# Kernel tuning notes

Measured on AMD Instinct MI355X. Metric: run time of the kernel, lower is better.

## Reference

```python
import jax, jax.numpy as jnp
import numpy as np

MARGIN1 = 0.5
ALPHA = 1.0
GAMMA = 1.0
THETA = 0.1
K = 8  # num_instances per identity

N = 4096
D_FEA = 512
N_CLS = 751
D_SIDE = 1024


def setup_inputs() -> dict:
    key = jax.random.key(0)
    ks = jax.random.split(key, 5)
    return {
        "cls_fea": jax.random.normal(ks[0], (N, N_CLS), dtype=jnp.float32),
        "l2_side": jax.random.normal(ks[1], (N, D_SIDE), dtype=jnp.float32),
        "l3_side": jax.random.normal(ks[2], (N, D_SIDE), dtype=jnp.float32),
        "l4_side": jax.random.normal(ks[3], (N, D_SIDE), dtype=jnp.float32),
        "input_fea": jax.random.normal(ks[4], (N, D_FEA), dtype=jnp.float32),
        # PK sampling: exactly K consecutive samples per identity
        "targets": jnp.arange(N, dtype=jnp.int32) // K,
    }


def _rank_terms(dist, mask, n):
    """Vectorized replacement of the per-row rank-mining python loop."""
    j = jnp.arange(n)
    k = jnp.arange(K)

    def row(drow, mrow):
        order = jnp.argsort(drow)          # ascending distances
        sd = drow[order]                   # sort_dist
        pm = mrow[order]                   # positive mask in rank order
        # negatives that sneaked into the top-K ranks (== full_index leftovers)
        flag_neg = (~pm) & (j < K)
        # positives ranked outside top-K (== wrong_indice)
        flag_pos = pm & (j >= K)
        m = jnp.sum(flag_neg)              # left_wrong_num (counts match by construction)
        # wrong negatives in ascending rank order, padded to K slots
        neg_ord = jnp.argsort(jnp.where(flag_neg, j, j + n))[:K]
        # wrong positives in DESCENDING rank order (loop iterates reverse-sorted)
        pos_ord = jnp.argsort(jnp.where(flag_pos, -j, 1))[:K]
        wneg = sd[neg_ord]
        wpos = sd[pos_ord]
        valid = k < m
        most_wrong_neg = wneg[0]           # smallest wrong-negative distance
        ratio = (most_wrong_neg - wneg) / (most_wrong_neg + 1e-12)
        weight = (m - k).astype(sd.dtype) * jnp.exp(ratio)
        loss = jnp.sum(jnp.where(valid, weight * (wpos - wneg) + MARGIN1, 0.0))
        return loss, (m == 0)

    return jax.vmap(row)(dist, mask)


def reference(cls_fea, l2_side, l3_side, l4_side, input_fea, targets):
    n = input_fea.shape[0]
    # pairwise euclidean distance, clamped like torch .clamp(min=1e-12).sqrt()
    sq = jnp.sum(input_fea * input_fea, axis=1)
    d2 = sq[:, None] + sq[None, :] - 2.0 * (input_fea @ input_fea.T)
    dist = jnp.sqrt(jnp.maximum(d2, 1e-12))
    mask = targets[:, None] == targets[None, :]

    losses, corrects = _rank_terms(dist, mask, n)
    rank_loss = jnp.sum(losses) / n
    prec = jnp.mean(corrects.astype(jnp.float32))

    # cross entropy
    logp = jax.nn.log_softmax(cls_fea, axis=-1)
    xent = -jnp.mean(jnp.take_along_axis(logp, targets[:, None].astype(jnp.int32), axis=1))

    # side losses: frobenius norms of differences
    side_loss = jnp.sqrt(jnp.sum((l4_side - l2_side) ** 2)) + \
                jnp.sqrt(jnp.sum((l4_side - l3_side) ** 2))

    total = ALPHA * rank_loss + GAMMA * xent + THETA * side_loss

    # accuracy() helper (undefined in source): standard top-1 on input_fea vs targets
    acc = jnp.mean((jnp.argmax(input_fea, axis=1).astype(targets.dtype) == targets).astype(jnp.float32))
    prec2 = jnp.maximum(prec, acc)
    return total, prec2
```

## Files before the change

kernel.cpp:

```cpp
#include <hip/hip_runtime.h>
#include <hip/hip_bf16.h>
#include <math.h>

#define NROWS 4096
#define DFEA  512
#define NCLS  751
#define DSIDE 1024

typedef __attribute__((ext_vector_type(8))) short short8;
typedef __attribute__((ext_vector_type(4))) float f32x4;

__device__ __forceinline__ float wave_sum(float v) {
#pragma unroll
  for (int off = 32; off > 0; off >>= 1) v += __shfl_xor(v, off, 64);
  return v;
}

__device__ __forceinline__ void load_lds16(const void* g, void* l) {
  __builtin_amdgcn_global_load_lds((const __attribute__((address_space(1))) void*)g,
                                   (__attribute__((address_space(3))) void*)l, 16, 0, 0);
}

__device__ __forceinline__ void ins8(float t8[8], float x) {
#pragma unroll
  for (int q = 0; q < 8; ++q) {
    const float lo = fminf(t8[q], x);
    x = fmaxf(t8[q], x);
    t8[q] = lo;
  }
}

#define CE(x, i, j) { const float ce_lo = fminf(x[i], x[j]); x[j] = fmaxf(x[i], x[j]); x[i] = ce_lo; }
#define SORT8_STAGE(c) \
  CE(c, 0, 4) CE(c, 1, 5) CE(c, 2, 6) CE(c, 3, 7) \
  CE(c, 0, 2) CE(c, 1, 3) CE(c, 4, 6) CE(c, 5, 7) \
  CE(c, 0, 1) CE(c, 2, 3) CE(c, 4, 5) CE(c, 6, 7)

__device__ __forceinline__ void merge_sorted8(float a[8], int mask) {
  float b[8];
#pragma unroll
  for (int i = 0; i < 8; ++i) b[i] = __shfl_xor(a[i], mask, 64);
  float c[8];
#pragma unroll
  for (int i = 0; i < 8; ++i) c[i] = fminf(a[i], b[7 - i]);
  SORT8_STAGE(c)
#pragma unroll
  for (int i = 0; i < 8; ++i) a[i] = c[i];
}

__device__ __forceinline__ void merge8_local(float a[8], const float b[8]) {
  float c[8];
#pragma unroll
  for (int i = 0; i < 8; ++i) c[i] = fminf(a[i], b[7 - i]);
  SORT8_STAGE(c)
#pragma unroll
  for (int i = 0; i < 8; ++i) a[i] = c[i];
}

__device__ __forceinline__ unsigned short bf16bits(float v) {
  union { __hip_bfloat16 b; unsigned short u; } cv;
  cv.b = __float2bfloat16(v);
  return cv.u;
}

__global__ __launch_bounds__(256) void k_prep(const float* __restrict__ fea,
                                              const int* __restrict__ tgt,
                                              float* __restrict__ sq,
                                              float* __restrict__ pa,
                                              unsigned short* __restrict__ Fhi,
                                              unsigned short* __restrict__ Flo) {
  const int lane = threadIdx.x & 63;
  const int wid  = threadIdx.x >> 6;
  const int row  = blockIdx.x * 4 + wid;
  const float4* xr = (const float4*)(fea + (size_t)row * DFEA);
  ushort4* hr = (ushort4*)(Fhi + (size_t)row * DFEA);
  ushort4* lr = (ushort4*)(Flo + (size_t)row * DFEA);
  float s = 0.0f, bv = -1e30f;
  int bi = 0;
#pragma unroll
  for (int q = 0; q < 2; ++q) {
    const int i4 = q * 64 + lane;
    const float4 v = xr[i4];
    s += v.x * v.x + v.y * v.y + v.z * v.z + v.w * v.w;
    const int c0 = i4 * 4;
    if (v.x > bv) { bv = v.x; bi = c0; }
    if (v.y > bv) { bv = v.y; bi = c0 + 1; }
    if (v.z > bv) { bv = v.z; bi = c0 + 2; }
    if (v.w > bv) { bv = v.w; bi = c0 + 3; }
    ushort4 h, l;
    float hf;
    h.x = bf16bits(v.x); hf = __bfloat162float(__ushort_as_bfloat16(h.x)); l.x = bf16bits(v.x - hf);
    h.y = bf16bits(v.y); hf = __bfloat162float(__ushort_as_bfloat16(h.y)); l.y = bf16bits(v.y - hf);
    h.z = bf16bits(v.z); hf = __bfloat162float(__ushort_as_bfloat16(h.z)); l.z = bf16bits(v.z - hf);
    h.w = bf16bits(v.w); hf = __bfloat162float(__ushort_as_bfloat16(h.w)); l.w = bf16bits(v.w - hf);
    hr[i4] = h;
    lr[i4] = l;
  }
#pragma unroll
  for (int off = 32; off > 0; off >>= 1) {
    s += __shfl_xor(s, off, 64);
    const float ov = __shfl_xor(bv, off, 64);
    const int   oi = __shfl_xor(bi, off, 64);
    if (ov > bv || (ov == bv && oi < bi)) { bv = ov; bi = oi; }
  }
  __shared__ float red[4];
  if (lane == 0) {
    sq[row]  = s;
    red[wid] = (bi == tgt[row]) ? 1.0f : 0.0f;
  }
  __syncthreads();
  if (threadIdx.x == 0) pa[blockIdx.x] = red[0] + red[1] + red[2] + red[3];
}

__global__ __launch_bounds__(256) void k_gemm_mfma(const unsigned short* __restrict__ Fhi,
                                                   const unsigned short* __restrict__ Flo,
                                                   const float* __restrict__ sq,
                                                   float* __restrict__ posw,
                                                   float* __restrict__ part) {
  const int bid = blockIdx.x;
  int by = (int)((65.0f - sqrtf(4225.0f - 8.0f * (float)bid)) * 0.5f);
  while ((by + 1) * (65 - (by + 1)) / 2 <= bid) ++by;
  while (by * (65 - by) / 2 > bid) --by;
  const int bx = by + (bid - by * (65 - by) / 2);

  const int R0 = by * 128, C0 = bx * 128;
  const int tid = threadIdx.x;
  const int lane = tid & 63, wid = tid >> 6;
  const int wr = wid >> 1, wc = wid & 1;
  const int l15 = lane & 15, l4 = lane >> 4;

  __shared__ __attribute__((aligned(16))) char smem[37376];
  const __hip_bfloat16 (*As)[64] = (const __hip_bfloat16(*)[64])smem;
  const __hip_bfloat16 (*Bs)[64] = (const __hip_bfloat16(*)[64])(smem + 16384);
  float (*dtile)[130] = (float(*)[130])smem;
  float* colb = (float*)(smem + 33280);

  f32x4 acc[4][4];
#pragma unroll
  for (int m = 0; m < 4; ++m)
#pragma unroll
    for (int n = 0; n < 4; ++n) acc[m][n] = (f32x4){0.0f, 0.0f, 0.0f, 0.0f};

  for (int kt = 0; kt < 24; ++kt) {
    const unsigned short* Aseg = (kt < 16) ? Fhi : Flo;
    const unsigned short* Bseg = (kt >= 8 && kt < 16) ? Flo : Fhi;
    const int ks = (kt & 7) * 64;
    __syncthreads();
#pragma unroll
    for (int i = 0; i < 4; ++i) {
      const int flat = i * 256 + tid;
      const int row = flat >> 3, c8 = flat & 7;
      load_lds16(Aseg + (size_t)(R0 + row) * DFEA + ks + c8 * 8,
                 smem + (i * 256 + wid * 64) * 16);
      load_lds16(Bseg + (size_t)(C0 + row) * DFEA + ks + c8 * 8,
                 smem + 16384 + (i * 256 + wid * 64) * 16);
    }
    __syncthreads();
#pragma unroll
    for (int kk = 0; kk < 2; ++kk) {
      short8 af[4], bf[4];
#pragma unroll
      for (int m = 0; m < 4; ++m)
        af[m] = *(const short8*)&As[wr * 64 + m * 16 + l15][kk * 32 + l4 * 8];
#pragma unroll
      for (int n = 0; n < 4; ++n)
        bf[n] = *(const short8*)&Bs[wc * 64 + n * 16 + l15][kk * 32 + l4 * 8];
#pragma unroll
      for (int m = 0; m < 4; ++m)
#pragma unroll
        for (int n = 0; n < 4; ++n)
          acc[m][n] = __builtin_amdgcn_mfma_f32_16x16x32_bf16(af[m], bf[n], acc[m][n], 0, 0, 0);
    }
  }

  float sqi[4][4], sqj[4];
#pragma unroll
  for (int m = 0; m < 4; ++m)
#pragma unroll
    for (int r = 0; r < 4; ++r) sqi[m][r] = sq[R0 + wr * 64 + m * 16 + l4 * 4 + r];
#pragma unroll
  for (int n = 0; n < 4; ++n) sqj[n] = sq[C0 + wc * 64 + n * 16 + l15];

  const bool diag = (bx == by);

  for (int h = 0; h < 2; ++h) {
    __syncthreads();
    if (wr == h) {
#pragma unroll
      for (int m = 0; m < 4; ++m)
#pragma unroll
        for (int n = 0; n < 4; ++n)
#pragma unroll
          for (int r = 0; r < 4; ++r)
            dtile[m * 16 + l4 * 4 + r][wc * 64 + n * 16 + l15] =
                sqi[m][r] + sqj[n] - 2.0f * acc[m][n][r];
    }
    __syncthreads();
    {
      const int r = tid >> 2, q = tid & 3;
      const int rg = R0 + h * 64 + r;
      float t8[8];
#pragma unroll
      for (int i = 0; i < 8; ++i) t8[i] = 1e30f;
      if (diag) {
        for (int s = 0; s < 32; ++s) {
          const int cl = q * 32 + ((s + 9 * q) & 31);
          const int cg = C0 + cl;
          const float v = dtile[r][cl];
          if (((rg ^ cg) >> 3) == 0) posw[(size_t)rg * 8 + (cg & 7)] = v;
          else if (v < t8[7]) ins8(t8, v);
        }
      } else {
        for (int s = 0; s < 32; ++s) {
          const float v = dtile[r][q * 32 + ((s + 9 * q) & 31)];
          if (v < t8[7]) ins8(t8, v);
        }
      }
      merge_sorted8(t8, 1);
      merge_sorted8(t8, 2);
      if (q == 0) {
        const float4 o0 = {t8[0], t8[1], t8[2], t8[3]};
        const float4 o1 = {t8[4], t8[5], t8[6], t8[7]};
        *(float4*)&part[(size_t)rg * 256 + bx * 8] = o0;
        *(float4*)&part[(size_t)rg * 256 + bx * 8 + 4] = o1;
      }
    }
    if (!diag) {
      const int c = tid >> 1, q2 = tid & 1;
      float c8[8];
#pragma unroll
      for (int i = 0; i < 8; ++i) c8[i] = 1e30f;
      for (int s = 0; s < 32; ++s) {
        const float v = dtile[q2 * 32 + s][c];
        if (v < c8[7]) ins8(c8, v);
      }
      merge_sorted8(c8, 1);
      if (q2 == 0) {
        if (h == 0) {
#pragma unroll
          for (int i = 0; i < 8; ++i) colb[c * 8 + i] = c8[i];
        } else {
          float o8[8];
#pragma unroll
          for (int i = 0; i < 8; ++i) o8[i] = colb[c * 8 + i];
          merge8_local(c8, o8);
          const int cg = C0 + c;
          const float4 o0 = {c8[0], c8[1], c8[2], c8[3]};
          const float4 o1 = {c8[4], c8[5], c8[6], c8[7]};
          *(float4*)&part[(size_t)cg * 256 + by * 8] = o0;
          *(float4*)&part[(size_t)cg * 256 + by * 8 + 4] = o1;
        }
      }
    }
  }
}

__global__ __launch_bounds__(256) void k_rank(const float* __restrict__ part,
                                              const float* __restrict__ posw,
                                              float* __restrict__ pl,
                                              float* __restrict__ pc) {
  const int lane = threadIdx.x & 63, w = threadIdx.x >> 6;
  const int row = blockIdx.x * 4 + w;
  float a[8];
  if (lane < 32) {
    const float4 v0 = *(const float4*)&part[(size_t)row * 256 + lane * 8];
    const float4 v1 = *(const float4*)&part[(size_t)row * 256 + lane * 8 + 4];
    a[0] = v0.x; a[1] = v0.y; a[2] = v0.z; a[3] = v0.w;
    a[4] = v1.x; a[5] = v1.y; a[6] = v1.z; a[7] = v1.w;
  } else {
#pragma unroll
    for (int i = 0; i < 8; ++i) a[i] = 1e30f;
  }
  merge_sorted8(a, 1);
  merge_sorted8(a, 2);
  merge_sorted8(a, 4);
  merge_sorted8(a, 8);
  merge_sorted8(a, 16);
  __shared__ float red[8];
  if (lane == 0) {
    float nd[8];
#pragma unroll
    for (int i = 0; i < 8; ++i) nd[i] = sqrtf(fmaxf(a[i], 1e-12f));
    float s8[8];
#pragma unroll
    for (int i = 0; i < 8; ++i) s8[i] = 1e30f;
#pragma unroll
    for (int i = 0; i < 8; ++i)
      ins8(s8, sqrtf(fmaxf(posw[(size_t)row * 8 + i], 1e-12f)));
    int ip = 0, in_ = 0;
#pragma unroll
    for (int s = 0; s < 8; ++s) {
      const bool takeNeg = (in_ < 8) && (ip >= 8 || nd[in_] < s8[ip]);
      if (takeNeg) ++in_; else ++ip;
    }
    const int m = in_;
    float loss = 0.0f;
    const float n0 = nd[0];
    for (int k = 0; k < m; ++k)
      loss += (float)(m - k) * expf((n0 - nd[k]) / (n0 + 1e-12f)) * (s8[7 - k] - nd[k]) + 0.5f;
    red[w] = loss;
    red[4 + w] = (m == 0) ? 1.0f : 0.0f;
  }
  __syncthreads();
  if (threadIdx.x == 0) {
    pl[blockIdx.x] = red[0] + red[1] + red[2] + red[3];
    pc[blockIdx.x] = red[4] + red[5] + red[6] + red[7];
  }
}

__global__ __launch_bounds__(256) void k_misc(const float* __restrict__ cls,
                                              const int* __restrict__ tgt,
                                              const float* __restrict__ l2,
                                              const float* __restrict__ l3,
                                              const float* __restrict__ l4,
                                              float* __restrict__ px,
                                              float* __restrict__ ps2,
                                              float* __restrict__ ps3) {
  const int lane = threadIdx.x & 63, wid = threadIdx.x >> 6;
  if (blockIdx.x < 1024) {
    const int row = blockIdx.x * 4 + wid;
    const float* x = cls + (size_t)row * NCLS;
    float mx = -1e30f;
    for (int c = lane; c < NCLS; c += 64) mx = fmaxf(mx, x[c]);
#pragma unroll
    for (int off = 32; off > 0; off >>= 1) mx = fmaxf(mx, __shfl_xor(mx, off, 64));
    float se = 0.0f;
    for (int c = lane; c < NCLS; c += 64) se += expf(x[c] - mx);
    se = wave_sum(se);
    __shared__ float redx[4];
    if (lane == 0) redx[wid] = logf(se) + mx - x[tgt[row]];
    __syncthreads();
    if (threadIdx.x == 0) px[blockIdx.x] = redx[0] + redx[1] + redx[2] + redx[3];
  } else {
    const int bid = blockIdx.x - 1024;
    float s2 = 0.0f, s3 = 0.0f;
    for (int i = bid * 256 + threadIdx.x; i < (NROWS * DSIDE / 4); i += 512 * 256) {
      const float4 a2 = ((const float4*)l2)[i];
      const float4 a3 = ((const float4*)l3)[i];
      const float4 a4 = ((const float4*)l4)[i];
      float dx = a4.x - a2.x, dy = a4.y - a2.y, dz = a4.z - a2.z, dw = a4.w - a2.w;
      s2 += dx * dx + dy * dy + dz * dz + dw * dw;
      dx = a4.x - a3.x; dy = a4.y - a3.y; dz = a4.z - a3.z; dw = a4.w - a3.w;
      s3 += dx * dx + dy * dy + dz * dz + dw * dw;
    }
    s2 = wave_sum(s2);
    s3 = wave_sum(s3);
    __shared__ float red[8];
    if (lane == 0) { red[wid] = s2; red[4 + wid] = s3; }
    __syncthreads();
    if (threadIdx.x == 0) {
      ps2[bid] = red[0] + red[1] + red[2] + red[3];
      ps3[bid] = red[4] + red[5] + red[6] + red[7];
    }
  }
}

__global__ __launch_bounds__(256) void k_fin(const float* __restrict__ pl,
                                             const float* __restrict__ pc,
                                             const float* __restrict__ px,
                                             const float* __restrict__ pa,
                                             const float* __restrict__ ps2,
                                             const float* __restrict__ ps3,
                                             float* __restrict__ out) {
  const int t = threadIdx.x;
  float s[6] = {0, 0, 0, 0, 0, 0};
  for (int i = t; i < 1024; i += 256) {
    s[0] += pl[i]; s[1] += pc[i]; s[2] += px[i]; s[3] += pa[i];
  }
  for (int i = t; i < 512; i += 256) {
    s[4] += ps2[i]; s[5] += ps3[i];
  }
  __shared__ float red[6][4];
  const int lane = t & 63, w = t >> 6;
#pragma unroll
  for (int j = 0; j < 6; ++j) {
    s[j] = wave_sum(s[j]);
    if (lane == 0) red[j][w] = s[j];
  }
  __syncthreads();
  if (t == 0) {
    const float rank_loss = (red[0][0] + red[0][1] + red[0][2] + red[0][3]) / (float)NROWS;
    const float prec      = (red[1][0] + red[1][1] + red[1][2] + red[1][3]) / (float)NROWS;
    const float xent      = (red[2][0] + red[2][1] + red[2][2] + red[2][3]) / (float)NROWS;
    const float acc       = (red[3][0] + red[3][1] + red[3][2] + red[3][3]) / (float)NROWS;
    const float side      = sqrtf(red[4][0] + red[4][1] + red[4][2] + red[4][3]) +
                            sqrtf(red[5][0] + red[5][1] + red[5][2] + red[5][3]);
    out[0] = rank_loss + xent + 0.1f * side;
    out[1] = fmaxf(prec, acc);
  }
}

extern "C" void kernel_launch(void* const* d_in, const int* in_sizes, int n_in,
                              void* d_out, int out_size, void* d_ws, size_t ws_size,
                              hipStream_t stream) {
  (void)in_sizes; (void)n_in; (void)out_size; (void)ws_size;
  const float* cls = (const float*)d_in[0];
  const float* l2  = (const float*)d_in[1];
  const float* l3  = (const float*)d_in[2];
  const float* l4  = (const float*)d_in[3];
  const float* fea = (const float*)d_in[4];
  const int*   tgt = (const int*)d_in[5];
  float* out = (float*)d_out;

  float* sq   = (float*)d_ws;
  unsigned short* Fhi = (unsigned short*)(sq + NROWS);
  unsigned short* Flo = Fhi + (size_t)NROWS * DFEA;
  float* part = (float*)(Flo + (size_t)NROWS * DFEA);
  float* posw = part + (size_t)NROWS * 256;
  float* pa   = posw + (size_t)NROWS * 8;
  float* pl   = pa + 1024;
  float* pc   = pl + 1024;
  float* px   = pc + 1024;
  float* ps2  = px + 1024;
  float* ps3  = ps2 + 512;

  k_prep<<<dim3(NROWS / 4), dim3(256), 0, stream>>>(fea, tgt, sq, pa, Fhi, Flo);
  k_gemm_mfma<<<dim3(528), dim3(256), 0, stream>>>(Fhi, Flo, sq, posw, part);
  k_rank<<<dim3(NROWS / 4), dim3(256), 0, stream>>>(part, posw, pl, pc);
  k_misc<<<dim3(1536), dim3(256), 0, stream>>>(cls, tgt, l2, l3, l4, px, ps2, ps3);
  k_fin<<<dim3(1), dim3(256), 0, stream>>>(pl, pc, px, pa, ps2, ps3, out);
}
```

Baseline: 222.6 us.

## Drop split-bf16 GEMM, compute full distance grid, fuse misc work into one kernel

```diff
diff --git a/kernel.cpp b/kernel.cpp
--- a/kernel.cpp
+++ b/kernel.cpp
@@ -48,15 +48,6 @@
   for (int i = 0; i < 8; ++i) a[i] = c[i];
 }
 
-__device__ __forceinline__ void merge8_local(float a[8], const float b[8]) {
-  float c[8];
-#pragma unroll
-  for (int i = 0; i < 8; ++i) c[i] = fminf(a[i], b[7 - i]);
-  SORT8_STAGE(c)
-#pragma unroll
-  for (int i = 0; i < 8; ++i) a[i] = c[i];
-}
-
 __device__ __forceinline__ unsigned short bf16bits(float v) {
   union { __hip_bfloat16 b; unsigned short u; } cv;
   cv.b = __float2bfloat16(v);
@@ -67,14 +58,12 @@
                                               const int* __restrict__ tgt,
                                               float* __restrict__ sq,
                                               float* __restrict__ pa,
-                                              unsigned short* __restrict__ Fhi,
-                                              unsigned short* __restrict__ Flo) {
+                                              unsigned short* __restrict__ Fhi) {
   const int lane = threadIdx.x & 63;
   const int wid  = threadIdx.x >> 6;
   const int row  = blockIdx.x * 4 + wid;
   const float4* xr = (const float4*)(fea + (size_t)row * DFEA);
   ushort4* hr = (ushort4*)(Fhi + (size_t)row * DFEA);
-  ushort4* lr = (ushort4*)(Flo + (size_t)row * DFEA);
   float s = 0.0f, bv = -1e30f;
   int bi = 0;
 #pragma unroll
@@ -87,14 +76,9 @@
     if (v.y > bv) { bv = v.y; bi = c0 + 1; }
     if (v.z > bv) { bv = v.z; bi = c0 + 2; }
     if (v.w > bv) { bv = v.w; bi = c0 + 3; }
-    ushort4 h, l;
-    float hf;
-    h.x = bf16bits(v.x); hf = __bfloat162float(__ushort_as_bfloat16(h.x)); l.x = bf16bits(v.x - hf);
-    h.y = bf16bits(v.y); hf = __bfloat162float(__ushort_as_bfloat16(h.y)); l.y = bf16bits(v.y - hf);
-    h.z = bf16bits(v.z); hf = __bfloat162float(__ushort_as_bfloat16(h.z)); l.z = bf16bits(v.z - hf);
-    h.w = bf16bits(v.w); hf = __bfloat162float(__ushort_as_bfloat16(h.w)); l.w = bf16bits(v.w - hf);
+    ushort4 h;
+    h.x = bf16bits(v.x); h.y = bf16bits(v.y); h.z = bf16bits(v.z); h.w = bf16bits(v.w);
     hr[i4] = h;
-    lr[i4] = l;
   }
 #pragma unroll
   for (int off = 32; off > 0; off >>= 1) {
@@ -112,91 +96,92 @@
   if (threadIdx.x == 0) pa[blockIdx.x] = red[0] + red[1] + red[2] + red[3];
 }
 
-__global__ __launch_bounds__(256) void k_gemm_mfma(const unsigned short* __restrict__ Fhi,
-                                                   const unsigned short* __restrict__ Flo,
-                                                   const float* __restrict__ sq,
-                                                   float* __restrict__ posw,
-                                                   float* __restrict__ part) {
+__global__ __launch_bounds__(256) void k_mega(const unsigned short* __restrict__ Fhi,
+                                              const float* __restrict__ sq,
+                                              float* __restrict__ posw,
+                                              float* __restrict__ part,
+                                              const float* __restrict__ cls,
+                                              const int* __restrict__ tgt,
+                                              const float* __restrict__ l2,
+                                              const float* __restrict__ l3,
+                                              const float* __restrict__ l4,
+                                              float* __restrict__ px,
+                                              float* __restrict__ ps2,
+                                              float* __restrict__ ps3) {
   const int bid = blockIdx.x;
-  int by = (int)((65.0f - sqrtf(4225.0f - 8.0f * (float)bid)) * 0.5f);
-  while ((by + 1) * (65 - (by + 1)) / 2 <= bid) ++by;
-  while (by * (65 - by) / 2 > bid) --by;
-  const int bx = by + (bid - by * (65 - by) / 2);
-
-  const int R0 = by * 128, C0 = bx * 128;
   const int tid = threadIdx.x;
   const int lane = tid & 63, wid = tid >> 6;
-  const int wr = wid >> 1, wc = wid & 1;
-  const int l15 = lane & 15, l4 = lane >> 4;
-
-  __shared__ __attribute__((aligned(16))) char smem[37376];
-  const __hip_bfloat16 (*As)[64] = (const __hip_bfloat16(*)[64])smem;
-  const __hip_bfloat16 (*Bs)[64] = (const __hip_bfloat16(*)[64])(smem + 16384);
-  float (*dtile)[130] = (float(*)[130])smem;
-  float* colb = (float*)(smem + 33280);
-
-  f32x4 acc[4][4];
-#pragma unroll
-  for (int m = 0; m < 4; ++m)
-#pragma unroll
-    for (int n = 0; n < 4; ++n) acc[m][n] = (f32x4){0.0f, 0.0f, 0.0f, 0.0f};
-
-  for (int kt = 0; kt < 24; ++kt) {
-    const unsigned short* Aseg = (kt < 16) ? Fhi : Flo;
-    const unsigned short* Bseg = (kt >= 8 && kt < 16) ? Flo : Fhi;
-    const int ks = (kt & 7) * 64;
-    __syncthreads();
-#pragma unroll
-    for (int i = 0; i < 4; ++i) {
-      const int flat = i * 256 + tid;
-      const int row = flat >> 3, c8 = flat & 7;
-      load_lds16(Aseg + (size_t)(R0 + row) * DFEA + ks + c8 * 8,
-                 smem + (i * 256 + wid * 64) * 16);
-      load_lds16(Bseg + (size_t)(C0 + row) * DFEA + ks + c8 * 8,
-                 smem + 16384 + (i * 256 + wid * 64) * 16);
-    }
-    __syncthreads();
-#pragma unroll
-    for (int kk = 0; kk < 2; ++kk) {
-      short8 af[4], bf[4];
-#pragma unroll
-      for (int m = 0; m < 4; ++m)
-        af[m] = *(const short8*)&As[wr * 64 + m * 16 + l15][kk * 32 + l4 * 8];
-#pragma unroll
-      for (int n = 0; n < 4; ++n)
-        bf[n] = *(const short8*)&Bs[wc * 64 + n * 16 + l15][kk * 32 + l4 * 8];
-#pragma unroll
-      for (int m = 0; m < 4; ++m)
+
+  if (bid < 1024) {
+    const int by = bid >> 5, bx = bid & 31;
+    const int R0 = by * 128, C0 = bx * 128;
+    const int wr = wid >> 1, wc = wid & 1;
+    const int l15 = lane & 15, l4 = lane >> 4;
+
+    __shared__ __attribute__((aligned(16))) char smem[33280];
+    const __hip_bfloat16 (*As)[64] = (const __hip_bfloat16(*)[64])smem;
+    const __hip_bfloat16 (*Bs)[64] = (const __hip_bfloat16(*)[64])(smem + 16384);
+    float (*dtile)[130] = (float(*)[130])smem;
+
+    f32x4 acc[4][4];
+#pragma unroll
+    for (int m = 0; m < 4; ++m)
+#pragma unroll
+      for (int n = 0; n < 4; ++n) acc[m][n] = (f32x4){0.0f, 0.0f, 0.0f, 0.0f};
+
+    for (int kt = 0; kt < 8; ++kt) {
+      const int ks = kt * 64;
+      __syncthreads();
+#pragma unroll
+      for (int i = 0; i < 4; ++i) {
+        const int flat = i * 256 + tid;
+        const int row = flat >> 3, c8 = flat & 7;
+        load_lds16(Fhi + (size_t)(R0 + row) * DFEA + ks + c8 * 8,
+                   smem + (i * 256 + wid * 64) * 16);
+        load_lds16(Fhi + (size_t)(C0 + row) * DFEA + ks + c8 * 8,
+                   smem + 16384 + (i * 256 + wid * 64) * 16);
+      }
+      __syncthreads();
+#pragma unroll
+      for (int kk = 0; kk < 2; ++kk) {
+        short8 af[4], bf[4];
+#pragma unroll
+        for (int m = 0; m < 4; ++m)
+          af[m] = *(const short8*)&As[wr * 64 + m * 16 + l15][kk * 32 + l4 * 8];
 #pragma unroll
         for (int n = 0; n < 4; ++n)
-          acc[m][n] = __builtin_amdgcn_mfma_f32_16x16x32_bf16(af[m], bf[n], acc[m][n], 0, 0, 0);
-    }
-  }
-
-  float sqi[4][4], sqj[4];
-#pragma unroll
-  for (int m = 0; m < 4; ++m)
-#pragma unroll
-    for (int r = 0; r < 4; ++r) sqi[m][r] = sq[R0 + wr * 64 + m * 16 + l4 * 4 + r];
-#pragma unroll
-  for (int n = 0; n < 4; ++n) sqj[n] = sq[C0 + wc * 64 + n * 16 + l15];
-
-  const bool diag = (bx == by);
-
-  for (int h = 0; h < 2; ++h) {
-    __syncthreads();
-    if (wr == h) {
-#pragma unroll
-      for (int m = 0; m < 4; ++m)
-#pragma unroll
-        for (int n = 0; n < 4; ++n)
-#pragma unroll
-          for (int r = 0; r < 4; ++r)
-            dtile[m * 16 + l4 * 4 + r][wc * 64 + n * 16 + l15] =
-                sqi[m][r] + sqj[n] - 2.0f * acc[m][n][r];
-    }
-    __syncthreads();
-    {
+          bf[n] = *(const short8*)&Bs[wc * 64 + n * 16 + l15][kk * 32 + l4 * 8];
+#pragma unroll
+        for (int m = 0; m < 4; ++m)
+#pragma unroll
+          for (int n = 0; n < 4; ++n)
+            acc[m][n] = __builtin_amdgcn_mfma_f32_16x16x32_bf16(af[m], bf[n], acc[m][n], 0, 0, 0);
+      }
+    }
+
+    float sqi[4][4], sqj[4];
+#pragma unroll
+    for (int m = 0; m < 4; ++m)
+#pragma unroll
+      for (int r = 0; r < 4; ++r) sqi[m][r] = sq[R0 + wr * 64 + m * 16 + l4 * 4 + r];
+#pragma unroll
+    for (int n = 0; n < 4; ++n) sqj[n] = sq[C0 + wc * 64 + n * 16 + l15];
+
+    const bool diag = (bx == by);
+
+    for (int h = 0; h < 2; ++h) {
+      __syncthreads();
+      if (wr == h) {
+#pragma unroll
+        for (int m = 0; m < 4; ++m)
+#pragma unroll
+          for (int n = 0; n < 4; ++n)
+#pragma unroll
+            for (int r = 0; r < 4; ++r)
+              dtile[m * 16 + l4 * 4 + r][wc * 64 + n * 16 + l15] =
+                  sqi[m][r] + sqj[n] - 2.0f * acc[m][n][r];
+      }
+      __syncthreads();
       const int r = tid >> 2, q = tid & 3;
       const int rg = R0 + h * 64 + r;
       float t8[8];
@@ -225,100 +210,8 @@
         *(float4*)&part[(size_t)rg * 256 + bx * 8 + 4] = o1;
       }
     }
-    if (!diag) {
-      const int c = tid >> 1, q2 = tid & 1;
-      float c8[8];
-#pragma unroll
-      for (int i = 0; i < 8; ++i) c8[i] = 1e30f;
-      for (int s = 0; s < 32; ++s) {
-        const float v = dtile[q2 * 32 + s][c];
-        if (v < c8[7]) ins8(c8, v);
-      }
-      merge_sorted8(c8, 1);
-      if (q2 == 0) {
-        if (h == 0) {
-#pragma unroll
-          for (int i = 0; i < 8; ++i) colb[c * 8 + i] = c8[i];
-        } else {
-          float o8[8];
-#pragma unroll
-          for (int i = 0; i < 8; ++i) o8[i] = colb[c * 8 + i];
-          merge8_local(c8, o8);
-          const int cg = C0 + c;
-          const float4 o0 = {c8[0], c8[1], c8[2], c8[3]};
-          const float4 o1 = {c8[4], c8[5], c8[6], c8[7]};
-          *(float4*)&part[(size_t)cg * 256 + by * 8] = o0;
-          *(float4*)&part[(size_t)cg * 256 + by * 8 + 4] = o1;
-        }
-      }
-    }
-  }
-}
-
-__global__ __launch_bounds__(256) void k_rank(const float* __restrict__ part,
-                                              const float* __restrict__ posw,
-                                              float* __restrict__ pl,
-                                              float* __restrict__ pc) {
-  const int lane = threadIdx.x & 63, w = threadIdx.x >> 6;
-  const int row = blockIdx.x * 4 + w;
-  float a[8];
-  if (lane < 32) {
-    const float4 v0 = *(const float4*)&part[(size_t)row * 256 + lane * 8];
-    const float4 v1 = *(const float4*)&part[(size_t)row * 256 + lane * 8 + 4];
-    a[0] = v0.x; a[1] = v0.y; a[2] = v0.z; a[3] = v0.w;
-    a[4] = v1.x; a[5] = v1.y; a[6] = v1.z; a[7] = v1.w;
-  } else {
-#pragma unroll
-    for (int i = 0; i < 8; ++i) a[i] = 1e30f;
-  }
-  merge_sorted8(a, 1);
-  merge_sorted8(a, 2);
-  merge_sorted8(a, 4);
-  merge_sorted8(a, 8);
-  merge_sorted8(a, 16);
-  __shared__ float red[8];
-  if (lane == 0) {
-    float nd[8];
-#pragma unroll
-    for (int i = 0; i < 8; ++i) nd[i] = sqrtf(fmaxf(a[i], 1e-12f));
-    float s8[8];
-#pragma unroll
-    for (int i = 0; i < 8; ++i) s8[i] = 1e30f;
-#pragma unroll
-    for (int i = 0; i < 8; ++i)
-      ins8(s8, sqrtf(fmaxf(posw[(size_t)row * 8 + i], 1e-12f)));
-    int ip = 0, in_ = 0;
-#pragma unroll
-    for (int s = 0; s < 8; ++s) {
-      const bool takeNeg = (in_ < 8) && (ip >= 8 || nd[in_] < s8[ip]);
-      if (takeNeg) ++in_; else ++ip;
-    }
-    const int m = in_;
-    float loss = 0.0f;
-    const float n0 = nd[0];
-    for (int k = 0; k < m; ++k)
-      loss += (float)(m - k) * expf((n0 - nd[k]) / (n0 + 1e-12f)) * (s8[7 - k] - nd[k]) + 0.5f;
-    red[w] = loss;
-    red[4 + w] = (m == 0) ? 1.0f : 0.0f;
-  }
-  __syncthreads();
-  if (threadIdx.x == 0) {
-    pl[blockIdx.x] = red[0] + red[1] + red[2] + red[3];
-    pc[blockIdx.x] = red[4] + red[5] + red[6] + red[7];
-  }
-}
-
-__global__ __launch_bounds__(256) void k_misc(const float* __restrict__ cls,
-                                              const int* __restrict__ tgt,
-                                              const float* __restrict__ l2,
-                                              const float* __restrict__ l3,
-                                              const float* __restrict__ l4,
-                                              float* __restrict__ px,
-                                              float* __restrict__ ps2,
-                                              float* __restrict__ ps3) {
-  const int lane = threadIdx.x & 63, wid = threadIdx.x >> 6;
-  if (blockIdx.x < 1024) {
-    const int row = blockIdx.x * 4 + wid;
+  } else if (bid < 2048) {
+    const int row = (bid - 1024) * 4 + wid;
     const float* x = cls + (size_t)row * NCLS;
     float mx = -1e30f;
     for (int c = lane; c < NCLS; c += 64) mx = fmaxf(mx, x[c]);
@@ -330,11 +223,11 @@
     __shared__ float redx[4];
     if (lane == 0) redx[wid] = logf(se) + mx - x[tgt[row]];
     __syncthreads();
-    if (threadIdx.x == 0) px[blockIdx.x] = redx[0] + redx[1] + redx[2] + redx[3];
+    if (tid == 0) px[bid - 1024] = redx[0] + redx[1] + redx[2] + redx[3];
   } else {
-    const int bid = blockIdx.x - 1024;
+    const int sb = bid - 2048;
     float s2 = 0.0f, s3 = 0.0f;
-    for (int i = bid * 256 + threadIdx.x; i < (NROWS * DSIDE / 4); i += 512 * 256) {
+    for (int i = sb * 256 + tid; i < (NROWS * DSIDE / 4); i += 512 * 256) {
       const float4 a2 = ((const float4*)l2)[i];
       const float4 a3 = ((const float4*)l3)[i];
       const float4 a4 = ((const float4*)l4)[i];
@@ -345,13 +238,65 @@
     }
     s2 = wave_sum(s2);
     s3 = wave_sum(s3);
-    __shared__ float red[8];
-    if (lane == 0) { red[wid] = s2; red[4 + wid] = s3; }
+    __shared__ float reds[8];
+    if (lane == 0) { reds[wid] = s2; reds[4 + wid] = s3; }
     __syncthreads();
-    if (threadIdx.x == 0) {
-      ps2[bid] = red[0] + red[1] + red[2] + red[3];
-      ps3[bid] = red[4] + red[5] + red[6] + red[7];
-    }
+    if (tid == 0) {
+      ps2[sb] = reds[0] + reds[1] + reds[2] + reds[3];
+      ps3[sb] = reds[4] + reds[5] + reds[6] + reds[7];
+    }
+  }
+}
+
+__global__ __launch_bounds__(256) void k_rank(const float* __restrict__ part,
+                                              const float* __restrict__ posw,
+                                              float* __restrict__ pl,
+                                              float* __restrict__ pc) {
+  const int lane = threadIdx.x & 63, w = threadIdx.x >> 6;
+  const int half = lane >> 5, l32 = lane & 31;
+  const int row = blockIdx.x * 8 + w * 2 + half;
+  float a[8];
+  const float4 v0 = *(const float4*)&part[(size_t)row * 256 + l32 * 8];
+  const float4 v1 = *(const float4*)&part[(size_t)row * 256 + l32 * 8 + 4];
+  a[0] = v0.x; a[1] = v0.y; a[2] = v0.z; a[3] = v0.w;
+  a[4] = v1.x; a[5] = v1.y; a[6] = v1.z; a[7] = v1.w;
+  merge_sorted8(a, 1);
+  merge_sorted8(a, 2);
+  merge_sorted8(a, 4);
+  merge_sorted8(a, 8);
+  merge_sorted8(a, 16);
+  __shared__ float red[16];
+  if (l32 == 0) {
+    float nd[8];
+#pragma unroll
+    for (int i = 0; i < 8; ++i) nd[i] = sqrtf(fmaxf(a[i], 1e-12f));
+    float s8[8];
+#pragma unroll
+    for (int i = 0; i < 8; ++i) s8[i] = 1e30f;
+#pragma unroll
+    for (int i = 0; i < 8; ++i)
+      ins8(s8, sqrtf(fmaxf(posw[(size_t)row * 8 + i], 1e-12f)));
+    int ip = 0, in_ = 0;
+#pragma unroll
+    for (int s = 0; s < 8; ++s) {
+      const bool takeNeg = (in_ < 8) && (ip >= 8 || nd[in_] < s8[ip]);
+      if (takeNeg) ++in_; else ++ip;
+    }
+    const int m = in_;
+    float loss = 0.0f;
+    const float n0 = nd[0];
+    for (int k = 0; k < m; ++k)
+      loss += (float)(m - k) * expf((n0 - nd[k]) / (n0 + 1e-12f)) * (s8[7 - k] - nd[k]) + 0.5f;
+    red[w * 2 + half] = loss;
+    red[8 + w * 2 + half] = (m == 0) ? 1.0f : 0.0f;
+  }
+  __syncthreads();
+  if (threadIdx.x == 0) {
+    float sl = 0.0f, sc = 0.0f;
+#pragma unroll
+    for (int i = 0; i < 8; ++i) { sl += red[i]; sc += red[8 + i]; }
+    pl[blockIdx.x] = sl;
+    pc[blockIdx.x] = sc;
   }
 }
 
@@ -364,11 +309,9 @@
                                              float* __restrict__ out) {
   const int t = threadIdx.x;
   float s[6] = {0, 0, 0, 0, 0, 0};
-  for (int i = t; i < 1024; i += 256) {
-    s[0] += pl[i]; s[1] += pc[i]; s[2] += px[i]; s[3] += pa[i];
-  }
+  for (int i = t; i < 1024; i += 256) { s[2] += px[i]; s[3] += pa[i]; }
   for (int i = t; i < 512; i += 256) {
-    s[4] += ps2[i]; s[5] += ps3[i];
+    s[0] += pl[i]; s[1] += pc[i]; s[4] += ps2[i]; s[5] += ps3[i];
   }
   __shared__ float red[6][4];
   const int lane = t & 63, w = t >> 6;
@@ -404,19 +347,18 @@
 
   float* sq   = (float*)d_ws;
   unsigned short* Fhi = (unsigned short*)(sq + NROWS);
-  unsigned short* Flo = Fhi + (size_t)NROWS * DFEA;
-  float* part = (float*)(Flo + (size_t)NROWS * DFEA);
+  float* part = (float*)(Fhi + (size_t)NROWS * DFEA);
   float* posw = part + (size_t)NROWS * 256;
   float* pa   = posw + (size_t)NROWS * 8;
   float* pl   = pa + 1024;
-  float* pc   = pl + 1024;
-  float* px   = pc + 1024;
+  float* pc   = pl + 512;
+  float* px   = pc + 512;
   float* ps2  = px + 1024;
   float* ps3  = ps2 + 512;
 
-  k_prep<<<dim3(NROWS / 4), dim3(256), 0, stream>>>(fea, tgt, sq, pa, Fhi, Flo);
-  k_gemm_mfma<<<dim3(528), dim3(256), 0, stream>>>(Fhi, Flo, sq, posw, part);
-  k_rank<<<dim3(NROWS / 4), dim3(256), 0, stream>>>(part, posw, pl, pc);
-  k_misc<<<dim3(1536), dim3(256), 0, stream>>>(cls, tgt, l2, l3, l4, px, ps2, ps3);
+  k_prep<<<dim3(NROWS / 4), dim3(256), 0, stream>>>(fea, tgt, sq, pa, Fhi);
+  k_mega<<<dim3(2560), dim3(256), 0, stream>>>(Fhi, sq, posw, part, cls, tgt, l2, l3, l4,
+                                               px, ps2, ps3);
+  k_rank<<<dim3(NROWS / 8), dim3(256), 0, stream>>>(part, posw, pl, pc);
   k_fin<<<dim3(1), dim3(256), 0, stream>>>(pl, pc, px, pa, ps2, ps3, out);
 }
```

New measurement: 180.9 us. 1.23x faster.
